# Kernel tuning notes

Measured on AMD Instinct MI355X. Metric: run time of the kernel, lower is better.

## Reference

```python
import jax, jax.numpy as jnp
import numpy as np

NEG_SLOPE = 0.2

def setup_inputs() -> dict:
    key = jax.random.key(0)
    k1, k2, k3 = jax.random.split(key, 3)
    x = jax.random.normal(k1, (4, 4096, 64), dtype=jnp.float32)
    weight_key = jax.random.normal(k2, (64, 1), dtype=jnp.float32)
    weight_query = jax.random.normal(k3, (64, 1), dtype=jnp.float32)
    return {"x": x, "weight_key": weight_key, "weight_query": weight_query}

def reference(x, weight_key, weight_query):
    # x: [bz, N, F]; key/query: [bz, N, 1]
    k = jnp.matmul(x, weight_key)          # [bz, N, 1]
    q = jnp.matmul(x, weight_query)        # [bz, N, 1]
    # additive broadcast attention: scores[b,i,j] = k[b,i] + q[b,j]
    scores = k + jnp.swapaxes(q, 1, 2)     # [bz, N, N]
    scores = jax.nn.leaky_relu(scores, negative_slope=NEG_SLOPE)
    attention = jax.nn.softmax(scores, axis=2)
    # dropout is identity in eval mode
    attn_feat = jnp.matmul(attention, x)   # [bz, N, F]
    return jnp.transpose(attn_feat, (0, 2, 1))  # [bz, F, N]
```

## Files before the change

kernel.cpp:

```cpp
#include <hip/hip_runtime.h>

#define N 4096
#define F 64
#define BZ 4

__device__ __forceinline__ unsigned int f2ord(float f) {
    unsigned int u = __float_as_uint(f);
    return (u & 0x80000000u) ? ~u : (u ^ 0x80000000u);
}
__device__ __forceinline__ float ord2f(unsigned int v) {
    unsigned int b = (v & 0x80000000u) ? (v ^ 0x80000000u) : ~v;
    return __uint_as_float(b);
}

__global__ __launch_bounds__(1024) void dot_kernel(
        const float* __restrict__ x, const float* __restrict__ wk,
        const float* __restrict__ wq, float* __restrict__ karr,
        unsigned long long* __restrict__ qkey, float* __restrict__ xT) {
    __shared__ float tile[64][68];
    const int b = blockIdx.x >> 6, chunk = blockIdx.x & 63;
    const int tid = threadIdx.x;
    const int wave = tid >> 6, lane = tid & 63;
    const int sub = lane >> 4, fq = lane & 15;
    const int lr = wave * 4 + sub;
    const int grow = chunk * 64 + lr;
    const int f0 = fq << 2;

    float4 xv = *(const float4*)(x + ((size_t)b * N + grow) * F + f0);
    float4 k4 = *(const float4*)(wk + f0);
    float4 q4 = *(const float4*)(wq + f0);
    float kk = xv.x * k4.x + xv.y * k4.y + xv.z * k4.z + xv.w * k4.w;
    float qq = xv.x * q4.x + xv.y * q4.y + xv.z * q4.z + xv.w * q4.w;
#pragma unroll
    for (int off = 1; off <= 8; off <<= 1) {
        kk += __shfl_xor(kk, off, 16);
        qq += __shfl_xor(qq, off, 16);
    }
    if (fq == 0) {
        karr[b * N + grow] = kk;
        qkey[b * N + grow] = ((unsigned long long)f2ord(qq) << 32)
                           | (unsigned int)grow;
    }
    tile[f0 + 0][lr] = xv.x;
    tile[f0 + 1][lr] = xv.y;
    tile[f0 + 2][lr] = xv.z;
    tile[f0 + 3][lr] = xv.w;
    __syncthreads();
    const int fo = wave * 4 + sub;
    float4 ov = *(const float4*)(&tile[fo][fq << 2]);
    *(float4*)(xT + ((size_t)(b * F + fo)) * N + chunk * 64 + (fq << 2)) = ov;
}

__global__ __launch_bounds__(1024) void rank_kernel(
        const unsigned long long* __restrict__ qkey,
        const float* __restrict__ karr,
        float* __restrict__ q_sorted, unsigned int* __restrict__ ordidx,
        int* __restrict__ pA) {
    __shared__ __align__(16) unsigned long long qs[N];
    __shared__ unsigned short pc[16][64];
    __shared__ unsigned short pc2[16][64];
    const int b = blockIdx.x >> 6, chunk = blockIdx.x & 63;
    const int tid = threadIdx.x;
    const int wave = tid >> 6, lane = tid & 63;
    const unsigned long long* qb = qkey + b * N;
    for (int t = tid; t < N; t += 1024) qs[t] = qb[t];
    const float kk = karr[b * N + chunk * 64 + lane];
    const unsigned int thetaOrd = f2ord(-kk);
    __syncthreads();

    const unsigned long long myKey = qs[chunk * 64 + lane];
    int cnt = 0, cnt2 = 0;
    const ulonglong2* q2 = (const ulonglong2*)qs;
    const int s0 = wave * 128;
#pragma unroll 8
    for (int t2 = 0; t2 < 128; ++t2) {
        ulonglong2 v = q2[s0 + t2];
        cnt  += (int)(v.x < myKey) + (int)(v.y < myKey);
        cnt2 += (int)((unsigned int)(v.x >> 32) < thetaOrd)
              + (int)((unsigned int)(v.y >> 32) < thetaOrd);
    }
    pc[wave][lane]  = (unsigned short)cnt;
    pc2[wave][lane] = (unsigned short)cnt2;
    __syncthreads();

    if (wave == 0) {
        int r = 0, p = 0;
#pragma unroll
        for (int w = 0; w < 16; ++w) { r += pc[w][lane]; p += pc2[w][lane]; }
        q_sorted[b * N + r] = ord2f((unsigned int)(myKey >> 32));
        ordidx[b * N + r] = (unsigned int)(myKey & 0xFFFFFFFFu);
        pA[b * N + chunk * 64 + lane] = p;
    }
}

__global__ __launch_bounds__(1024) void feat_kernel(
        const float* __restrict__ xT, const float* __restrict__ karr,
        const float* __restrict__ q_sorted,
        const unsigned int* __restrict__ ordidx,
        const int* __restrict__ pA, float* __restrict__ out) {
    __shared__ __align__(16) float SUF1[N + 4], PRE2[N + 4];
    __shared__ __align__(16) float SUFD[N + 4], PRED[N + 4];
    __shared__ float wt1[16], wt2[16], wtd1[16], wtd2[16];
    __shared__ float wb1[16], wb2[16], wbd1[16], wbd2[16];
    const int bid = blockIdx.x;
    const int b = bid >> 6, f = bid & 63;
    const int tid = threadIdx.x;
    const int wave = tid >> 6, lane = tid & 63;
    const int t0 = tid << 2;
    const float* qsb = q_sorted + b * N;
    const float Qmax = qsb[N - 1];

    float4 qv = *(const float4*)(qsb + t0);
    uint4 iv = *(const uint4*)(ordidx + b * N + t0);
    float qa[4] = {qv.x, qv.y, qv.z, qv.w};
    unsigned ia[4] = {iv.x, iv.y, iv.z, iv.w};
    float e1[4], e2[4], w1[4], w2[4];
    const float* xrow = xT + (size_t)(b * F + f) * N;
#pragma unroll
    for (int r = 0; r < 4; ++r) {
        float d = qa[r] - Qmax;
        e1[r] = __expf(d);
        e2[r] = __expf(0.2f * d);
        float xf = xrow[ia[r]];
        w1[r] = e1[r] * xf;
        w2[r] = e2[r] * xf;
    }

    float lp2_0 = 0.f, lp2_1 = w2[0], lp2_2 = lp2_1 + w2[1], lp2_3 = lp2_2 + w2[2];
    float T2 = lp2_3 + w2[3];
    float lpd_0 = 0.f, lpd_1 = e2[0], lpd_2 = lpd_1 + e2[1], lpd_3 = lpd_2 + e2[2];
    float TD2 = lpd_3 + e2[3];
    float ls1_3 = w1[3], ls1_2 = w1[2] + ls1_3, ls1_1 = w1[1] + ls1_2, ls1_0 = w1[0] + ls1_1;
    float T1 = ls1_0;
    float lsd_3 = e1[3], lsd_2 = e1[2] + lsd_3, lsd_1 = e1[1] + lsd_2, lsd_0 = e1[0] + lsd_1;
    float TD1 = lsd_0;

    float ip2 = T2, ipd2 = TD2;
#pragma unroll
    for (int d = 1; d < 64; d <<= 1) {
        float n1 = __shfl_up(ip2, d, 64);
        float n2 = __shfl_up(ipd2, d, 64);
        if (lane >= d) { ip2 += n1; ipd2 += n2; }
    }
    float is1 = T1, isd1 = TD1;
#pragma unroll
    for (int d = 1; d < 64; d <<= 1) {
        float n1 = __shfl_down(is1, d, 64);
        float n2 = __shfl_down(isd1, d, 64);
        if (lane + d < 64) { is1 += n1; isd1 += n2; }
    }
    if (lane == 63) { wt2[wave] = ip2; wtd2[wave] = ipd2; }
    if (lane == 0)  { wt1[wave] = is1; wtd1[wave] = isd1; }
    __syncthreads();
    if (tid == 0) {
        float a2 = 0.f, ad2 = 0.f;
#pragma unroll
        for (int w = 0; w < 16; ++w) {
            wb2[w] = a2; a2 += wt2[w];
            wbd2[w] = ad2; ad2 += wtd2[w];
        }
        PRE2[N] = a2; PRED[N] = ad2;
        float a1 = 0.f, ad1 = 0.f;
#pragma unroll
        for (int w = 15; w >= 0; --w) {
            wb1[w] = a1; a1 += wt1[w];
            wbd1[w] = ad1; ad1 += wtd1[w];
        }
        SUF1[N] = 0.f; SUFD[N] = 0.f;
    }
    __syncthreads();
    float bp2 = wb2[wave] + (ip2 - T2);
    float bpd = wbd2[wave] + (ipd2 - TD2);
    float bs1 = wb1[wave] + (is1 - T1);
    float bsd = wbd1[wave] + (isd1 - TD1);
    float4 o;
    o.x = bp2 + lp2_0; o.y = bp2 + lp2_1; o.z = bp2 + lp2_2; o.w = bp2 + lp2_3;
    *(float4*)(PRE2 + t0) = o;
    o.x = bpd + lpd_0; o.y = bpd + lpd_1; o.z = bpd + lpd_2; o.w = bpd + lpd_3;
    *(float4*)(PRED + t0) = o;
    o.x = bs1 + ls1_0; o.y = bs1 + ls1_1; o.z = bs1 + ls1_2; o.w = bs1 + ls1_3;
    *(float4*)(SUF1 + t0) = o;
    o.x = bsd + lsd_0; o.y = bsd + lsd_1; o.z = bsd + lsd_2; o.w = bsd + lsd_3;
    *(float4*)(SUFD + t0) = o;
    __syncthreads();

    float4 kv = *(const float4*)(karr + b * N + t0);
    int4 pv = *(const int4*)(pA + b * N + t0);
    float ka[4] = {kv.x, kv.y, kv.z, kv.w};
    int pa[4] = {pv.x, pv.y, pv.z, pv.w};
    float ra[4];
#pragma unroll
    for (int r = 0; r < 4; ++r) {
        float kk = ka[r];
        int p = pa[r];
        float u = kk + Qmax;
        float M = fmaxf(u, 0.2f * u);
        float c1 = __expf(u - M);
        float c2 = __expf(0.2f * u - M);
        float num = c1 * SUF1[p] + c2 * PRE2[p];
        float den = c1 * SUFD[p] + c2 * PRED[p];
        ra[r] = num / den;
    }
    float4 res; res.x = ra[0]; res.y = ra[1]; res.z = ra[2]; res.w = ra[3];
    *(float4*)(out + ((size_t)(b * F + f)) * N + t0) = res;
}

extern "C" void kernel_launch(void* const* d_in, const int* in_sizes, int n_in,
                              void* d_out, int out_size, void* d_ws, size_t ws_size,
                              hipStream_t stream) {
    const float* x  = (const float*)d_in[0];
    const float* wk = (const float*)d_in[1];
    const float* wq = (const float*)d_in[2];
    float* out = (float*)d_out;

    float* ws = (float*)d_ws;
    float* karr = ws;
    unsigned long long* qkey = (unsigned long long*)(ws + BZ * N);
    float* q_sorted = ws + 3 * BZ * N;
    unsigned int* ordidx = (unsigned int*)(ws + 4 * BZ * N);
    int* pA = (int*)(ws + 5 * BZ * N);
    float* xT = ws + 6 * BZ * N;

    dot_kernel<<<BZ * 64, 1024, 0, stream>>>(x, wk, wq, karr, qkey, xT);
    rank_kernel<<<BZ * 64, 1024, 0, stream>>>(qkey, karr, q_sorted, ordidx, pA);
    feat_kernel<<<BZ * F, 1024, 0, stream>>>(xT, karr, q_sorted, ordidx, pA, out);
}
```

Before: 78.49 us.

## Fuse three kernels into one persistent kernel with device-wide flag barriers

Merges the dot/transpose, rank and feature kernels into a single 256-block launch that uses atomic flag arrays as grid-wide barriers between the phases, so two kernel launch gaps disappear. It also passes k from shared memory, replaces the serial tid==0 block-offset scan with 16-lane shuffle scans, and clamps indices defensively. The grid barrier depends on all 256 blocks of 1024 threads being resident at once, and the flag reset protocol across calls is fragile. Spinning and the agent-scope fences add their own cost.

```diff
diff --git a/kernel.cpp b/kernel.cpp
--- a/kernel.cpp
+++ b/kernel.cpp
@@ -3,6 +3,8 @@
 #define N 4096
 #define F 64
 #define BZ 4
+#define MAGIC1 0x1F2E3D4Cu
+#define MAGIC2 0x5A6B7C8Du
 
 __device__ __forceinline__ unsigned int f2ord(float f) {
     unsigned int u = __float_as_uint(f);
@@ -13,196 +15,248 @@
     return __uint_as_float(b);
 }
 
-__global__ __launch_bounds__(1024) void dot_kernel(
+__device__ __forceinline__ void dev_barrier(unsigned* flags, unsigned magic,
+                                            int bid, int tid, int wave, int lane) {
+    __syncthreads();
+    if (tid == 0) {
+        __builtin_amdgcn_fence(__ATOMIC_RELEASE, "agent");
+        __hip_atomic_store(flags + bid, magic, __ATOMIC_RELAXED,
+                           __HIP_MEMORY_SCOPE_AGENT);
+    }
+    if (wave == 0) {
+        for (;;) {
+            unsigned a0 = __hip_atomic_load(flags + lane, __ATOMIC_RELAXED,
+                                            __HIP_MEMORY_SCOPE_AGENT);
+            unsigned a1 = __hip_atomic_load(flags + 64 + lane, __ATOMIC_RELAXED,
+                                            __HIP_MEMORY_SCOPE_AGENT);
+            unsigned a2 = __hip_atomic_load(flags + 128 + lane, __ATOMIC_RELAXED,
+                                            __HIP_MEMORY_SCOPE_AGENT);
+            unsigned a3 = __hip_atomic_load(flags + 192 + lane, __ATOMIC_RELAXED,
+                                            __HIP_MEMORY_SCOPE_AGENT);
+            bool ok = (a0 == magic) & (a1 == magic) & (a2 == magic) & (a3 == magic);
+            if (__all(ok)) break;
+            __builtin_amdgcn_s_sleep(2);
+        }
+        __builtin_amdgcn_fence(__ATOMIC_ACQUIRE, "agent");
+    }
+    __syncthreads();
+    asm volatile("" ::: "memory");
+}
+
+__global__ __launch_bounds__(1024) void fused_gat(
         const float* __restrict__ x, const float* __restrict__ wk,
-        const float* __restrict__ wq, float* __restrict__ karr,
-        unsigned long long* __restrict__ qkey, float* __restrict__ xT) {
-    __shared__ float tile[64][68];
-    const int b = blockIdx.x >> 6, chunk = blockIdx.x & 63;
+        const float* __restrict__ wq, unsigned* __restrict__ flags1,
+        unsigned* __restrict__ flags2, float* __restrict__ karr,
+        unsigned long long* __restrict__ qkey, float* __restrict__ q_sorted,
+        unsigned int* __restrict__ ordidx, int* __restrict__ pA,
+        float* __restrict__ xT, float* __restrict__ out) {
+    __shared__ __align__(16) char smem[66176];
+    const int bid = blockIdx.x;
     const int tid = threadIdx.x;
     const int wave = tid >> 6, lane = tid & 63;
-    const int sub = lane >> 4, fq = lane & 15;
-    const int lr = wave * 4 + sub;
-    const int grow = chunk * 64 + lr;
-    const int f0 = fq << 2;
-
-    float4 xv = *(const float4*)(x + ((size_t)b * N + grow) * F + f0);
-    float4 k4 = *(const float4*)(wk + f0);
-    float4 q4 = *(const float4*)(wq + f0);
-    float kk = xv.x * k4.x + xv.y * k4.y + xv.z * k4.z + xv.w * k4.w;
-    float qq = xv.x * q4.x + xv.y * q4.y + xv.z * q4.z + xv.w * q4.w;
-#pragma unroll
-    for (int off = 1; off <= 8; off <<= 1) {
-        kk += __shfl_xor(kk, off, 16);
-        qq += __shfl_xor(qq, off, 16);
-    }
-    if (fq == 0) {
-        karr[b * N + grow] = kk;
-        qkey[b * N + grow] = ((unsigned long long)f2ord(qq) << 32)
-                           | (unsigned int)grow;
-    }
-    tile[f0 + 0][lr] = xv.x;
-    tile[f0 + 1][lr] = xv.y;
-    tile[f0 + 2][lr] = xv.z;
-    tile[f0 + 3][lr] = xv.w;
-    __syncthreads();
-    const int fo = wave * 4 + sub;
-    float4 ov = *(const float4*)(&tile[fo][fq << 2]);
-    *(float4*)(xT + ((size_t)(b * F + fo)) * N + chunk * 64 + (fq << 2)) = ov;
-}
-
-__global__ __launch_bounds__(1024) void rank_kernel(
-        const unsigned long long* __restrict__ qkey,
-        const float* __restrict__ karr,
-        float* __restrict__ q_sorted, unsigned int* __restrict__ ordidx,
-        int* __restrict__ pA) {
-    __shared__ __align__(16) unsigned long long qs[N];
-    __shared__ unsigned short pc[16][64];
-    __shared__ unsigned short pc2[16][64];
-    const int b = blockIdx.x >> 6, chunk = blockIdx.x & 63;
-    const int tid = threadIdx.x;
-    const int wave = tid >> 6, lane = tid & 63;
-    const unsigned long long* qb = qkey + b * N;
-    for (int t = tid; t < N; t += 1024) qs[t] = qb[t];
-    const float kk = karr[b * N + chunk * 64 + lane];
-    const unsigned int thetaOrd = f2ord(-kk);
-    __syncthreads();
-
-    const unsigned long long myKey = qs[chunk * 64 + lane];
-    int cnt = 0, cnt2 = 0;
-    const ulonglong2* q2 = (const ulonglong2*)qs;
-    const int s0 = wave * 128;
+    const int b = bid >> 6, chunk = bid & 63;
+
+    float* kks = (float*)(smem + 36864);
+
+    if (tid == 0)
+        __hip_atomic_store(flags2 + bid, 0u, __ATOMIC_RELAXED,
+                           __HIP_MEMORY_SCOPE_AGENT);
+
+    {
+        float (*tile)[68] = (float(*)[68])smem;
+        const int row = tid >> 4;
+        const int fq = tid & 15;
+        const int grow = (chunk << 6) + row;
+        const int f0 = fq << 2;
+        float4 xv = *(const float4*)(x + ((size_t)b * N + grow) * F + f0);
+        float4 k4 = *(const float4*)(wk + f0);
+        float4 q4 = *(const float4*)(wq + f0);
+        float kk = xv.x * k4.x + xv.y * k4.y + xv.z * k4.z + xv.w * k4.w;
+        float qq = xv.x * q4.x + xv.y * q4.y + xv.z * q4.z + xv.w * q4.w;
+#pragma unroll
+        for (int off = 1; off <= 8; off <<= 1) {
+            kk += __shfl_xor(kk, off, 16);
+            qq += __shfl_xor(qq, off, 16);
+        }
+        if (fq == 0) {
+            kks[row] = kk;
+            karr[b * N + grow] = kk;
+            qkey[b * N + grow] = ((unsigned long long)f2ord(qq) << 32)
+                               | (unsigned int)grow;
+        }
+        tile[f0 + 0][row] = xv.x;
+        tile[f0 + 1][row] = xv.y;
+        tile[f0 + 2][row] = xv.z;
+        tile[f0 + 3][row] = xv.w;
+        __syncthreads();
+        const int fo = row;
+        float4 ov = *(const float4*)(&tile[fo][fq << 2]);
+        *(float4*)(xT + ((size_t)(b * F + fo)) * N + (chunk << 6) + (fq << 2)) = ov;
+    }
+    dev_barrier(flags1, MAGIC1, bid, tid, wave, lane);
+
+    {
+        unsigned long long* qs = (unsigned long long*)smem;
+        unsigned short (*pc)[64] = (unsigned short(*)[64])(smem + 32768);
+        unsigned short (*pc2)[64] = (unsigned short(*)[64])(smem + 34816);
+        const unsigned long long* qb = qkey + b * N;
+        for (int t = tid; t < N; t += 1024) qs[t] = qb[t];
+        const float kk = kks[lane];
+        const unsigned int thetaOrd = f2ord(-kk);
+        __syncthreads();
+
+        const unsigned long long myKey = qs[(chunk << 6) + lane];
+        int cnt = 0, cnt2 = 0;
+        const ulonglong2* q2 = (const ulonglong2*)qs;
+        const int s0 = wave * 128;
 #pragma unroll 8
-    for (int t2 = 0; t2 < 128; ++t2) {
-        ulonglong2 v = q2[s0 + t2];
-        cnt  += (int)(v.x < myKey) + (int)(v.y < myKey);
-        cnt2 += (int)((unsigned int)(v.x >> 32) < thetaOrd)
-              + (int)((unsigned int)(v.y >> 32) < thetaOrd);
-    }
-    pc[wave][lane]  = (unsigned short)cnt;
-    pc2[wave][lane] = (unsigned short)cnt2;
-    __syncthreads();
-
-    if (wave == 0) {
-        int r = 0, p = 0;
-#pragma unroll
-        for (int w = 0; w < 16; ++w) { r += pc[w][lane]; p += pc2[w][lane]; }
-        q_sorted[b * N + r] = ord2f((unsigned int)(myKey >> 32));
-        ordidx[b * N + r] = (unsigned int)(myKey & 0xFFFFFFFFu);
-        pA[b * N + chunk * 64 + lane] = p;
-    }
-}
-
-__global__ __launch_bounds__(1024) void feat_kernel(
-        const float* __restrict__ xT, const float* __restrict__ karr,
-        const float* __restrict__ q_sorted,
-        const unsigned int* __restrict__ ordidx,
-        const int* __restrict__ pA, float* __restrict__ out) {
-    __shared__ __align__(16) float SUF1[N + 4], PRE2[N + 4];
-    __shared__ __align__(16) float SUFD[N + 4], PRED[N + 4];
-    __shared__ float wt1[16], wt2[16], wtd1[16], wtd2[16];
-    __shared__ float wb1[16], wb2[16], wbd1[16], wbd2[16];
-    const int bid = blockIdx.x;
-    const int b = bid >> 6, f = bid & 63;
-    const int tid = threadIdx.x;
-    const int wave = tid >> 6, lane = tid & 63;
-    const int t0 = tid << 2;
-    const float* qsb = q_sorted + b * N;
-    const float Qmax = qsb[N - 1];
-
-    float4 qv = *(const float4*)(qsb + t0);
-    uint4 iv = *(const uint4*)(ordidx + b * N + t0);
-    float qa[4] = {qv.x, qv.y, qv.z, qv.w};
-    unsigned ia[4] = {iv.x, iv.y, iv.z, iv.w};
-    float e1[4], e2[4], w1[4], w2[4];
-    const float* xrow = xT + (size_t)(b * F + f) * N;
-#pragma unroll
-    for (int r = 0; r < 4; ++r) {
-        float d = qa[r] - Qmax;
-        e1[r] = __expf(d);
-        e2[r] = __expf(0.2f * d);
-        float xf = xrow[ia[r]];
-        w1[r] = e1[r] * xf;
-        w2[r] = e2[r] * xf;
-    }
-
-    float lp2_0 = 0.f, lp2_1 = w2[0], lp2_2 = lp2_1 + w2[1], lp2_3 = lp2_2 + w2[2];
-    float T2 = lp2_3 + w2[3];
-    float lpd_0 = 0.f, lpd_1 = e2[0], lpd_2 = lpd_1 + e2[1], lpd_3 = lpd_2 + e2[2];
-    float TD2 = lpd_3 + e2[3];
-    float ls1_3 = w1[3], ls1_2 = w1[2] + ls1_3, ls1_1 = w1[1] + ls1_2, ls1_0 = w1[0] + ls1_1;
-    float T1 = ls1_0;
-    float lsd_3 = e1[3], lsd_2 = e1[2] + lsd_3, lsd_1 = e1[1] + lsd_2, lsd_0 = e1[0] + lsd_1;
-    float TD1 = lsd_0;
-
-    float ip2 = T2, ipd2 = TD2;
-#pragma unroll
-    for (int d = 1; d < 64; d <<= 1) {
-        float n1 = __shfl_up(ip2, d, 64);
-        float n2 = __shfl_up(ipd2, d, 64);
-        if (lane >= d) { ip2 += n1; ipd2 += n2; }
-    }
-    float is1 = T1, isd1 = TD1;
-#pragma unroll
-    for (int d = 1; d < 64; d <<= 1) {
-        float n1 = __shfl_down(is1, d, 64);
-        float n2 = __shfl_down(isd1, d, 64);
-        if (lane + d < 64) { is1 += n1; isd1 += n2; }
-    }
-    if (lane == 63) { wt2[wave] = ip2; wtd2[wave] = ipd2; }
-    if (lane == 0)  { wt1[wave] = is1; wtd1[wave] = isd1; }
-    __syncthreads();
-    if (tid == 0) {
-        float a2 = 0.f, ad2 = 0.f;
-#pragma unroll
-        for (int w = 0; w < 16; ++w) {
-            wb2[w] = a2; a2 += wt2[w];
-            wbd2[w] = ad2; ad2 += wtd2[w];
-        }
-        PRE2[N] = a2; PRED[N] = ad2;
-        float a1 = 0.f, ad1 = 0.f;
-#pragma unroll
-        for (int w = 15; w >= 0; --w) {
-            wb1[w] = a1; a1 += wt1[w];
-            wbd1[w] = ad1; ad1 += wtd1[w];
-        }
-        SUF1[N] = 0.f; SUFD[N] = 0.f;
-    }
-    __syncthreads();
-    float bp2 = wb2[wave] + (ip2 - T2);
-    float bpd = wbd2[wave] + (ipd2 - TD2);
-    float bs1 = wb1[wave] + (is1 - T1);
-    float bsd = wbd1[wave] + (isd1 - TD1);
-    float4 o;
-    o.x = bp2 + lp2_0; o.y = bp2 + lp2_1; o.z = bp2 + lp2_2; o.w = bp2 + lp2_3;
-    *(float4*)(PRE2 + t0) = o;
-    o.x = bpd + lpd_0; o.y = bpd + lpd_1; o.z = bpd + lpd_2; o.w = bpd + lpd_3;
-    *(float4*)(PRED + t0) = o;
-    o.x = bs1 + ls1_0; o.y = bs1 + ls1_1; o.z = bs1 + ls1_2; o.w = bs1 + ls1_3;
-    *(float4*)(SUF1 + t0) = o;
-    o.x = bsd + lsd_0; o.y = bsd + lsd_1; o.z = bsd + lsd_2; o.w = bsd + lsd_3;
-    *(float4*)(SUFD + t0) = o;
-    __syncthreads();
-
-    float4 kv = *(const float4*)(karr + b * N + t0);
-    int4 pv = *(const int4*)(pA + b * N + t0);
-    float ka[4] = {kv.x, kv.y, kv.z, kv.w};
-    int pa[4] = {pv.x, pv.y, pv.z, pv.w};
-    float ra[4];
-#pragma unroll
-    for (int r = 0; r < 4; ++r) {
-        float kk = ka[r];
-        int p = pa[r];
-        float u = kk + Qmax;
-        float M = fmaxf(u, 0.2f * u);
-        float c1 = __expf(u - M);
-        float c2 = __expf(0.2f * u - M);
-        float num = c1 * SUF1[p] + c2 * PRE2[p];
-        float den = c1 * SUFD[p] + c2 * PRED[p];
-        ra[r] = num / den;
-    }
-    float4 res; res.x = ra[0]; res.y = ra[1]; res.z = ra[2]; res.w = ra[3];
-    *(float4*)(out + ((size_t)(b * F + f)) * N + t0) = res;
+        for (int t2 = 0; t2 < 128; ++t2) {
+            ulonglong2 v = q2[s0 + t2];
+            cnt  += (int)(v.x < myKey) + (int)(v.y < myKey);
+            cnt2 += (int)((unsigned int)(v.x >> 32) < thetaOrd)
+                  + (int)((unsigned int)(v.y >> 32) < thetaOrd);
+        }
+        pc[wave][lane]  = (unsigned short)cnt;
+        pc2[wave][lane] = (unsigned short)cnt2;
+        __syncthreads();
+
+        if (wave == 0) {
+            int r = 0, p = 0;
+#pragma unroll
+            for (int w = 0; w < 16; ++w) { r += pc[w][lane]; p += pc2[w][lane]; }
+            q_sorted[b * N + r] = ord2f((unsigned int)(myKey >> 32));
+            ordidx[b * N + r] = (unsigned int)(myKey & 0xFFFFFFFFu);
+            pA[b * N + (chunk << 6) + lane] = p;
+        }
+    }
+    dev_barrier(flags2, MAGIC2, bid, tid, wave, lane);
+
+    {
+        const int f = chunk;
+        float* SUF1 = (float*)smem;
+        float* PRE2 = (float*)(smem + 16416);
+        float* SUFD = (float*)(smem + 32832);
+        float* PRED = (float*)(smem + 49248);
+        float* wt1  = (float*)(smem + 65664);
+        float* wtd1 = (float*)(smem + 65728);
+        float* wt2  = (float*)(smem + 65792);
+        float* wtd2 = (float*)(smem + 65856);
+        float* wb1  = (float*)(smem + 65920);
+        float* wbd1 = (float*)(smem + 65984);
+        float* wb2  = (float*)(smem + 66048);
+        float* wbd2 = (float*)(smem + 66112);
+        const int t0 = tid << 2;
+        const float* qsb = q_sorted + b * N;
+        const float Qmax = qsb[N - 1];
+
+        float4 qv = *(const float4*)(qsb + t0);
+        uint4 iv = *(const uint4*)(ordidx + b * N + t0);
+        float qa[4] = {qv.x, qv.y, qv.z, qv.w};
+        unsigned ia[4] = {iv.x & (N - 1), iv.y & (N - 1),
+                          iv.z & (N - 1), iv.w & (N - 1)};
+        float e1[4], e2[4], w1[4], w2[4];
+        const float* xrow = xT + (size_t)(b * F + f) * N;
+#pragma unroll
+        for (int r = 0; r < 4; ++r) {
+            float d = qa[r] - Qmax;
+            e1[r] = __expf(d);
+            e2[r] = __expf(0.2f * d);
+            float xf = xrow[ia[r]];
+            w1[r] = e1[r] * xf;
+            w2[r] = e2[r] * xf;
+        }
+
+        float lp2_0 = 0.f, lp2_1 = w2[0], lp2_2 = lp2_1 + w2[1], lp2_3 = lp2_2 + w2[2];
+        float T2 = lp2_3 + w2[3];
+        float lpd_0 = 0.f, lpd_1 = e2[0], lpd_2 = lpd_1 + e2[1], lpd_3 = lpd_2 + e2[2];
+        float TD2 = lpd_3 + e2[3];
+        float ls1_3 = w1[3], ls1_2 = w1[2] + ls1_3, ls1_1 = w1[1] + ls1_2, ls1_0 = w1[0] + ls1_1;
+        float T1 = ls1_0;
+        float lsd_3 = e1[3], lsd_2 = e1[2] + lsd_3, lsd_1 = e1[1] + lsd_2, lsd_0 = e1[0] + lsd_1;
+        float TD1 = lsd_0;
+
+        float ip2 = T2, ipd2 = TD2;
+#pragma unroll
+        for (int d = 1; d < 64; d <<= 1) {
+            float n1 = __shfl_up(ip2, d, 64);
+            float n2 = __shfl_up(ipd2, d, 64);
+            if (lane >= d) { ip2 += n1; ipd2 += n2; }
+        }
+        float is1 = T1, isd1 = TD1;
+#pragma unroll
+        for (int d = 1; d < 64; d <<= 1) {
+            float n1 = __shfl_down(is1, d, 64);
+            float n2 = __shfl_down(isd1, d, 64);
+            if (lane + d < 64) { is1 += n1; isd1 += n2; }
+        }
+        if (lane == 63) { wt2[wave] = ip2; wtd2[wave] = ipd2; }
+        if (lane == 0)  { wt1[wave] = is1; wtd1[wave] = isd1; }
+        __syncthreads();
+        if (wave == 0 && lane < 16) {
+            float v = wt2[lane], vd = wtd2[lane];
+            float s = v, sd = vd;
+#pragma unroll
+            for (int d = 1; d < 16; d <<= 1) {
+                float n1 = __shfl_up(s, d, 64);
+                float n2 = __shfl_up(sd, d, 64);
+                if (lane >= d) { s += n1; sd += n2; }
+            }
+            wb2[lane] = s - v; wbd2[lane] = sd - vd;
+            if (lane == 15) { PRE2[N] = s; PRED[N] = sd; }
+        }
+        if (wave == 1 && lane < 16) {
+            float v = wt1[lane], vd = wtd1[lane];
+            float s = v, sd = vd;
+#pragma unroll
+            for (int d = 1; d < 16; d <<= 1) {
+                float n1 = __shfl_down(s, d, 64);
+                float n2 = __shfl_down(sd, d, 64);
+                if (lane + d < 16) { s += n1; sd += n2; }
+            }
+            wb1[lane] = s - v; wbd1[lane] = sd - vd;
+            if (lane == 0) { SUF1[N] = 0.f; SUFD[N] = 0.f; }
+        }
+        __syncthreads();
+        float bp2 = wb2[wave] + (ip2 - T2);
+        float bpd = wbd2[wave] + (ipd2 - TD2);
+        float bs1 = wb1[wave] + (is1 - T1);
+        float bsd = wbd1[wave] + (isd1 - TD1);
+        float4 o;
+        o.x = bp2 + lp2_0; o.y = bp2 + lp2_1; o.z = bp2 + lp2_2; o.w = bp2 + lp2_3;
+        *(float4*)(PRE2 + t0) = o;
+        o.x = bpd + lpd_0; o.y = bpd + lpd_1; o.z = bpd + lpd_2; o.w = bpd + lpd_3;
+        *(float4*)(PRED + t0) = o;
+        o.x = bs1 + ls1_0; o.y = bs1 + ls1_1; o.z = bs1 + ls1_2; o.w = bs1 + ls1_3;
+        *(float4*)(SUF1 + t0) = o;
+        o.x = bsd + lsd_0; o.y = bsd + lsd_1; o.z = bsd + lsd_2; o.w = bsd + lsd_3;
+        *(float4*)(SUFD + t0) = o;
+        __syncthreads();
+
+        float4 kv = *(const float4*)(karr + b * N + t0);
+        int4 pv = *(const int4*)(pA + b * N + t0);
+        float ka[4] = {kv.x, kv.y, kv.z, kv.w};
+        int pa[4] = {pv.x, pv.y, pv.z, pv.w};
+        float ra[4];
+#pragma unroll
+        for (int r = 0; r < 4; ++r) {
+            float kk = ka[r];
+            int p = pa[r];
+            if ((unsigned)p > N) p = N;
+            float u = kk + Qmax;
+            float M = fmaxf(u, 0.2f * u);
+            float c1 = __expf(u - M);
+            float c2 = __expf(0.2f * u - M);
+            float num = c1 * SUF1[p] + c2 * PRE2[p];
+            float den = c1 * SUFD[p] + c2 * PRED[p];
+            ra[r] = num / den;
+        }
+        float4 res; res.x = ra[0]; res.y = ra[1]; res.z = ra[2]; res.w = ra[3];
+        *(float4*)(out + ((size_t)(b * F + f)) * N + t0) = res;
+    }
+
+    if (tid == 0)
+        __hip_atomic_store(flags1 + bid, 0u, __ATOMIC_RELAXED,
+                           __HIP_MEMORY_SCOPE_AGENT);
 }
 
 extern "C" void kernel_launch(void* const* d_in, const int* in_sizes, int n_in,
@@ -213,15 +267,16 @@
     const float* wq = (const float*)d_in[2];
     float* out = (float*)d_out;
 
-    float* ws = (float*)d_ws;
-    float* karr = ws;
-    unsigned long long* qkey = (unsigned long long*)(ws + BZ * N);
-    float* q_sorted = ws + 3 * BZ * N;
-    unsigned int* ordidx = (unsigned int*)(ws + 4 * BZ * N);
-    int* pA = (int*)(ws + 5 * BZ * N);
-    float* xT = ws + 6 * BZ * N;
-
-    dot_kernel<<<BZ * 64, 1024, 0, stream>>>(x, wk, wq, karr, qkey, xT);
-    rank_kernel<<<BZ * 64, 1024, 0, stream>>>(qkey, karr, q_sorted, ordidx, pA);
-    feat_kernel<<<BZ * F, 1024, 0, stream>>>(xT, karr, q_sorted, ordidx, pA, out);
-}
+    float* wsf = (float*)d_ws;
+    unsigned* flags1 = (unsigned*)wsf;
+    unsigned* flags2 = flags1 + 256;
+    float* karr = wsf + 512;
+    unsigned long long* qkey = (unsigned long long*)(wsf + 512 + BZ * N);
+    float* q_sorted = wsf + 512 + 3 * BZ * N;
+    unsigned int* ordidx = (unsigned int*)(wsf + 512 + 4 * BZ * N);
+    int* pA = (int*)(wsf + 512 + 5 * BZ * N);
+    float* xT = wsf + 512 + 6 * BZ * N;
+
+    fused_gat<<<BZ * 64, 1024, 0, stream>>>(x, wk, wq, flags1, flags2, karr,
+                                            qkey, q_sorted, ordidx, pA, xT, out);
+}
```

After: 100.4 us. +27.9%, slower.
